# Kernel tuning notes

Hardware: AMD Instinct MI355X
Metric: run time of the kernel (lower is better)

Reference implementation:

```python
import jax, jax.numpy as jnp
import numpy as np

B, N, BS, H, DH, L, FF, V, R = 1, 4096, 64, 12, 64, 4, 3072, 30522, 3
D = H * DH
M = N // BS
NEG = -10000.0


def layernorm(x, g, b, eps=1e-5):
    mu = x.mean(-1, keepdims=True)
    var = ((x - mu) ** 2).mean(-1, keepdims=True)
    return (x - mu) * jax.lax.rsqrt(var + eps) * g + b


def bigbird_attention(q, k, v, band_mask, from_mask, to_mask, blocked_mask, rand_attn):
    # q,k,v: [b,h,n,d]; band_mask [b,1,m-4,BS,3BS]; to_mask [b,1,1,n]; from_mask [b,1,n,1]
    b, h, n, d = q.shape
    m = n // BS
    r = rand_attn.shape[-1]
    sc = 1.0 / jnp.sqrt(jnp.float32(d))
    qb = q.reshape(b, h, m, BS, d)
    kb = k.reshape(b, h, m, BS, d)
    vb = v.reshape(b, h, m, BS, d)
    hid = jnp.arange(h)[:, None, None]
    gk = kb[:, hid, rand_attn].reshape(b, h, m - 2, r * BS, d)  # gathered random keys
    gv = vb[:, hid, rand_attn].reshape(b, h, m - 2, r * BS, d)
    rand_to = blocked_mask[:, rand_attn].reshape(b, h, m - 2, r * BS)
    rand_mask = jnp.einsum('blq,bhlk->bhlqk', blocked_mask[:, 1:-1], rand_to)  # [b,h,m-2,BS,rBS]

    # first block: dense over all keys (global)
    s = jnp.einsum('bhqd,bhkd->bhqk', qb[:, :, 0], k) * sc + (1.0 - to_mask) * NEG
    c_first = jnp.einsum('bhqk,bhkd->bhqd', jax.nn.softmax(s, axis=-1), v)

    # second block: blocks 0,1,2, last, + random row 0
    k2 = jnp.concatenate([kb[:, :, 0], kb[:, :, 1], kb[:, :, 2], kb[:, :, -1], gk[:, :, 0]], axis=2)
    v2 = jnp.concatenate([vb[:, :, 0], vb[:, :, 1], vb[:, :, 2], vb[:, :, -1], gv[:, :, 0]], axis=2)
    s = jnp.einsum('bhqd,bhkd->bhqk', qb[:, :, 1], k2) * sc
    seq_pad = jnp.concatenate([to_mask[..., :3 * BS], to_mask[..., -BS:],
                               jnp.ones((b, 1, 1, r * BS), s.dtype)], axis=3)
    rnd_pad = jnp.concatenate([jnp.ones((b, h, BS, 4 * BS), s.dtype), rand_mask[:, :, 0]], axis=3)
    s = s + (1.0 - jnp.minimum(seq_pad, rnd_pad)) * NEG
    c_second = jnp.einsum('bhqk,bhkd->bhqd', jax.nn.softmax(s, axis=-1), v2)

    # middle blocks: first-global + 3-block band + random + last-global
    mq = qb[:, :, 2:-2]  # [b,h,m-4,BS,d]
    exp_k = jnp.concatenate([kb[:, :, 1:-3], kb[:, :, 2:-2], kb[:, :, 3:-1]], axis=3)
    exp_v = jnp.concatenate([vb[:, :, 1:-3], vb[:, :, 2:-2], vb[:, :, 3:-1]], axis=3)
    inner = jnp.einsum('bhlqd,bhlkd->bhlqk', mq, exp_k) * sc + (1.0 - band_mask) * NEG
    randp = jnp.einsum('bhlqd,bhlkd->bhlqk', mq, gk[:, :, 1:-1]) * sc + (1.0 - rand_mask[:, :, 1:-1]) * NEG
    firstp = jnp.einsum('bhlqd,bhkd->bhlqk', mq, kb[:, :, 0]) * sc + (1.0 - to_mask[:, :, None, :, :BS]) * NEG
    lastp = jnp.einsum('bhlqd,bhkd->bhlqk', mq, kb[:, :, -1]) * sc + (1.0 - to_mask[:, :, None, :, -BS:]) * NEG
    w = jax.nn.softmax(jnp.concatenate([firstp, inner, randp, lastp], axis=-1), axis=-1)
    c_mid = jnp.einsum('bhlqk,bhlkd->bhlqd', w[..., BS:4 * BS], exp_v)
    c_mid = c_mid + jnp.einsum('bhlqk,bhlkd->bhlqd', w[..., 4 * BS:4 * BS + r * BS], gv[:, :, 1:-1])
    c_mid = c_mid + jnp.einsum('bhlqk,bhkd->bhlqd', w[..., :BS], vb[:, :, 0])
    c_mid = c_mid + jnp.einsum('bhlqk,bhkd->bhlqd', w[..., -BS:], vb[:, :, -1])

    # second-to-last block: block 0, last 3 blocks, + random row -1
    k3 = jnp.concatenate([kb[:, :, 0], kb[:, :, -3], kb[:, :, -2], kb[:, :, -1], gk[:, :, -1]], axis=2)
    v3 = jnp.concatenate([vb[:, :, 0], vb[:, :, -3], vb[:, :, -2], vb[:, :, -1], gv[:, :, -1]], axis=2)
    s = jnp.einsum('bhqd,bhkd->bhqk', qb[:, :, -2], k3) * sc
    seq_pad = jnp.concatenate([to_mask[..., :BS], to_mask[..., -3 * BS:],
                               jnp.ones((b, 1, 1, r * BS), s.dtype)], axis=3)
    rnd_pad = jnp.concatenate([jnp.ones((b, h, BS, 4 * BS), s.dtype), rand_mask[:, :, -1]], axis=3)
    s = s + (1.0 - jnp.minimum(seq_pad, rnd_pad)) * NEG
    c_sl = jnp.einsum('bhqk,bhkd->bhqd', jax.nn.softmax(s, axis=-1), v3)

    # last block: dense over all keys (global)
    s = jnp.einsum('bhqd,bhkd->bhqk', qb[:, :, -1], k) * sc + (1.0 - to_mask) * NEG
    c_last = jnp.einsum('bhqk,bhkd->bhqd', jax.nn.softmax(s, axis=-1), v)

    ctx = jnp.concatenate([c_first[:, :, None], c_second[:, :, None], c_mid,
                           c_sl[:, :, None], c_last[:, :, None]], axis=2)
    ctx = ctx.reshape(b, h, n, d) * from_mask
    return ctx.transpose(0, 2, 1, 3).reshape(b, n, h * d)


def forward(input_ids, mask, rand_attn, emb_word, emb_pos, emb_ln_g, emb_ln_b,
            Wq, bq, Wk, bk, Wv, bv, Wo, bo, ln1_g, ln1_b, W1, b1, W2, b2, ln2_g, ln2_b):
    b, n = input_ids.shape
    m = n // BS
    x = emb_word[input_ids] + emb_pos[None, :n]
    x = layernorm(x, emb_ln_g, emb_ln_b)
    blocked_mask = mask.reshape(b, m, BS)
    exp_to = jnp.concatenate([blocked_mask[:, 1:-3], blocked_mask[:, 2:-2], blocked_mask[:, 3:-1]], axis=2)
    band_mask = jnp.einsum('blq,blk->blqk', blocked_mask[:, 2:-2], exp_to)[:, None]
    from_mask = mask.reshape(b, 1, n, 1)
    to_mask = mask.reshape(b, 1, 1, n)
    for i in range(L):
        q = (x @ Wq[i] + bq[i]).reshape(b, n, H, DH).transpose(0, 2, 1, 3)
        k = (x @ Wk[i] + bk[i]).reshape(b, n, H, DH).transpose(0, 2, 1, 3)
        v = (x @ Wv[i] + bv[i]).reshape(b, n, H, DH).transpose(0, 2, 1, 3)
        a = bigbird_attention(q, k, v, band_mask, from_mask, to_mask, blocked_mask, rand_attn)
        a = a @ Wo[i] + bo[i]
        x = layernorm(x + a, ln1_g[i], ln1_b[i])  # dropout is identity in eval
        f = jax.nn.gelu(x @ W1[i] + b1[i], approximate=False) @ W2[i] + b2[i]
        x = layernorm(x + f, ln2_g[i], ln2_b[i])
    return x


def setup_inputs() -> dict:
    key = jax.random.key(0)
    ks = jax.random.split(key, 12)
    s = 0.02
    nrm = lambda k, shape: jax.random.normal(k, shape, jnp.float32) * s
    rng = np.random.default_rng(0)
    rand_attn = jnp.asarray(rng.integers(1, M - 1, size=(H, M - 2, R)), jnp.int32)
    return {
        'input_ids': jax.random.randint(ks[0], (B, N), 0, V),
        'mask': jnp.ones((B, N), jnp.float32),
        'rand_attn': rand_attn,
        'emb_word': nrm(ks[1], (V, D)),
        'emb_pos': nrm(ks[2], (N, D)),
        'emb_ln_g': jnp.ones((D,), jnp.float32), 'emb_ln_b': jnp.zeros((D,), jnp.float32),
        'Wq': nrm(ks[3], (L, D, D)), 'bq': jnp.zeros((L, D), jnp.float32),
        'Wk': nrm(ks[4], (L, D, D)), 'bk': jnp.zeros((L, D), jnp.float32),
        'Wv': nrm(ks[5], (L, D, D)), 'bv': jnp.zeros((L, D), jnp.float32),
        'Wo': nrm(ks[6], (L, D, D)), 'bo': jnp.zeros((L, D), jnp.float32),
        'ln1_g': jnp.ones((L, D), jnp.float32), 'ln1_b': jnp.zeros((L, D), jnp.float32),
        'W1': nrm(ks[7], (L, D, FF)), 'b1': jnp.zeros((L, FF), jnp.float32),
        'W2': nrm(ks[8], (L, FF, D)), 'b2': jnp.zeros((L, D), jnp.float32),
        'ln2_g': jnp.ones((L, D), jnp.float32), 'ln2_b': jnp.zeros((L, D), jnp.float32),
    }


def reference(input_ids, mask, rand_attn, emb_word, emb_pos, emb_ln_g, emb_ln_b,
              Wq, bq, Wk, bk, Wv, bv, Wo, bo, ln1_g, ln1_b, W1, b1, W2, b2, ln2_g, ln2_b):
    return forward(input_ids, mask, rand_attn, emb_word, emb_pos, emb_ln_g, emb_ln_b,
                   Wq, bq, Wk, bk, Wv, bv, Wo, bo, ln1_g, ln1_b, W1, b1, W2, b2, ln2_g, ln2_b)
```

## Files before the change

### kernel.cpp

```cpp
#include <hip/hip_runtime.h>
#include <hip/hip_bf16.h>
#include <math.h>

#define NTOK   4096
#define DMODEL 768
#define NHEAD  12
#define DHEAD  64
#define NLAYER 4
#define DFF    3072
#define NBLK   64
#define NEGC   -10000.0f

using frag8 = __attribute__((ext_vector_type(8))) short;
using f32x4 = __attribute__((ext_vector_type(4))) float;

typedef __attribute__((address_space(3))) void       lds_void;
typedef const __attribute__((address_space(1))) void gbl_void;

__device__ __forceinline__ void gload_lds16(const void* g, void* l) {
  __builtin_amdgcn_global_load_lds((gbl_void*)g, (lds_void*)l, 16, 0, 0);
}

__device__ __forceinline__ float block_sum256(float v) {
  __shared__ float tmp[4];
  #pragma unroll
  for (int o = 32; o > 0; o >>= 1) v += __shfl_down(v, o, 64);
  __syncthreads();
  if ((threadIdx.x & 63) == 0) tmp[threadIdx.x >> 6] = v;
  __syncthreads();
  return tmp[0] + tmp[1] + tmp[2] + tmp[3];
}

__global__ __launch_bounds__(256) void embed_ln_kernel(
    const int* __restrict__ ids, const float* __restrict__ emb_word,
    const float* __restrict__ emb_pos, const float* __restrict__ g,
    const float* __restrict__ b, float* __restrict__ x,
    __hip_bfloat16* __restrict__ xb)
{
  const int n = blockIdx.x;
  const int tid = threadIdx.x;
  const int id = ids[n];
  float v[3];
  #pragma unroll
  for (int j = 0; j < 3; ++j) {
    int d = tid + j * 256;
    v[j] = emb_word[(size_t)id * DMODEL + d] + emb_pos[(size_t)n * DMODEL + d];
  }
  float mu = block_sum256(v[0] + v[1] + v[2]) * (1.0f / DMODEL);
  float var = 0.f;
  #pragma unroll
  for (int j = 0; j < 3; ++j) { float t = v[j] - mu; var += t * t; }
  var = block_sum256(var) * (1.0f / DMODEL);
  float rs = rsqrtf(var + 1e-5f);
  #pragma unroll
  for (int j = 0; j < 3; ++j) {
    int d = tid + j * 256;
    float o = (v[j] - mu) * rs * g[d] + b[d];
    x[(size_t)n * DMODEL + d] = o;
    xb[(size_t)n * DMODEL + d] = (__hip_bfloat16)o;
  }
}

__global__ __launch_bounds__(256) void add_ln_red_kernel(
    const float* __restrict__ xin, const float* __restrict__ P, size_t ps,
    int nparts, const float* __restrict__ bias2,
    const float* __restrict__ g, const float* __restrict__ b,
    float* __restrict__ dst, __hip_bfloat16* __restrict__ dstb)
{
  const int n = blockIdx.x;
  const int tid = threadIdx.x;
  float v[3];
  #pragma unroll
  for (int j = 0; j < 3; ++j) {
    int d = tid + j * 256;
    float s = xin[(size_t)n * DMODEL + d] + bias2[d];
    for (int z = 0; z < nparts; ++z)
      s += P[(size_t)z * ps + (size_t)n * DMODEL + d];
    v[j] = s;
  }
  float mu = block_sum256(v[0] + v[1] + v[2]) * (1.0f / DMODEL);
  float var = 0.f;
  #pragma unroll
  for (int j = 0; j < 3; ++j) { float t = v[j] - mu; var += t * t; }
  var = block_sum256(var) * (1.0f / DMODEL);
  float rs = rsqrtf(var + 1e-5f);
  #pragma unroll
  for (int j = 0; j < 3; ++j) {
    int d = tid + j * 256;
    float ov = (v[j] - mu) * rs * g[d] + b[d];
    dst[(size_t)n * DMODEL + d] = ov;
    dstb[(size_t)n * DMODEL + d] = (__hip_bfloat16)ov;
  }
}

__global__ __launch_bounds__(256) void prep_weights_kernel(
    const float* __restrict__ Wq, const float* __restrict__ Wk,
    const float* __restrict__ Wv, const float* __restrict__ Wo,
    const float* __restrict__ W1, const float* __restrict__ W2,
    const float* __restrict__ bq, const float* __restrict__ bk,
    const float* __restrict__ bv,
    __hip_bfloat16* __restrict__ wqkvT, __hip_bfloat16* __restrict__ woT,
    __hip_bfloat16* __restrict__ w1T, __hip_bfloat16* __restrict__ w2T,
    float* __restrict__ biasf)
{
  const int id = blockIdx.x;
  if (id >= 6912) {
    int t = (id - 6912) * 256 + threadIdx.x;
    if (t < 3 * DMODEL)
      biasf[t] = (t < DMODEL) ? bq[t] : (t < 2 * DMODEL ? bk[t - DMODEL] : bv[t - 2 * DMODEL]);
    return;
  }
  const float* src;
  __hip_bfloat16* dst;
  int K, N, local;
  if (id < 2304) {
    int m = id / 576; local = id % 576;
    src = (m == 0) ? Wq : (m == 1) ? Wk : (m == 2) ? Wv : Wo;
    dst = (m < 3) ? wqkvT + (size_t)m * DMODEL * DMODEL : woT;
    K = DMODEL; N = DMODEL;
  } else if (id < 4608) {
    local = id - 2304; src = W1; dst = w1T; K = DMODEL; N = DFF;
  } else {
    local = id - 4608; src = W2; dst = w2T; K = DFF; N = DMODEL;
  }
  const int ntiles = N / 32;
  const int n0 = (local % ntiles) * 32;
  const int k0 = (local / ntiles) * 32;

  __shared__ float tile[32][33];
  const int c = threadIdx.x & 31;
  const int r0 = threadIdx.x >> 5;
  #pragma unroll
  for (int i = 0; i < 4; ++i) {
    int r = r0 + i * 8;
    tile[r][c] = src[(size_t)(k0 + r) * N + n0 + c];
  }
  __syncthreads();
  #pragma unroll
  for (int i = 0; i < 4; ++i) {
    int r = r0 + i * 8;
    dst[(size_t)(n0 + r) * K + k0 + c] = (__hip_bfloat16)tile[c][r];
  }
}

__global__ __launch_bounds__(256) void gemm_bf16_kernel(
    const __hip_bfloat16* __restrict__ A, int lda,
    const __hip_bfloat16* __restrict__ BT, int ldb,
    const float* __restrict__ bias,
    float* __restrict__ Cf, size_t cfStride,
    __hip_bfloat16* __restrict__ Cb,
    int Kpart, int ldC, int do_gelu)
{
  __shared__ __hip_bfloat16 Als[2][64 * 32];
  __shared__ __hip_bfloat16 Bls[2][128 * 32];
  const int tid = threadIdx.x;

  const int gx = gridDim.x;
  const int nwg = gx * gridDim.y;
  const int orig = blockIdx.y * gx + blockIdx.x;
  const int q = nwg >> 3, r = nwg & 7;
  const int xcd = orig & 7, loc = orig >> 3;
  const int wg = (xcd < r ? xcd * (q + 1) : r * (q + 1) + (xcd - r) * q) + loc;
  const int bm = (wg % gx) * 64;
  const int bn = (wg / gx) * 128;
  const int z  = blockIdx.z;
  const int koff = z * Kpart;

  const int wave = tid >> 6, lane = tid & 63;
  const int wm = (wave >> 1) * 32, wn = (wave & 1) * 64;
  const int lm = lane & 15, quad = lane >> 4;

  const int rA = wave * 16 + (lane >> 2);
  const int kc = (lane & 3) * 8;

  const __hip_bfloat16* Ar  = A  + (size_t)(bm + rA) * lda + koff + kc;
  const __hip_bfloat16* Br0 = BT + (size_t)(bn + rA) * ldb + koff + kc;
  const __hip_bfloat16* Br1 = BT + (size_t)(bn + 64 + rA) * ldb + koff + kc;

  f32x4 acc[2][4];
  #pragma unroll
  for (int i = 0; i < 2; ++i)
    #pragma unroll
    for (int j = 0; j < 4; ++j)
      acc[i][j] = (f32x4){0.f, 0.f, 0.f, 0.f};

  gload_lds16(Ar,  &Als[0][rA * 32 + kc]);
  gload_lds16(Br0, &Bls[0][rA * 32 + kc]);
  gload_lds16(Br1, &Bls[0][(64 + rA) * 32 + kc]);

  int p = 0;
  for (int k0 = 0; k0 < Kpart; k0 += 32, p ^= 1) {
    __syncthreads();
    const int kn = k0 + 32;
    if (kn < Kpart) {
      gload_lds16(Ar + kn,  &Als[p ^ 1][rA * 32 + kc]);
      gload_lds16(Br0 + kn, &Bls[p ^ 1][rA * 32 + kc]);
      gload_lds16(Br1 + kn, &Bls[p ^ 1][(64 + rA) * 32 + kc]);
    }
    frag8 afr[2], bfr[4];
    #pragma unroll
    for (int t = 0; t < 2; ++t)
      afr[t] = *(const frag8*)(&Als[p][(wm + t * 16 + lm) * 32 + quad * 8]);
    #pragma unroll
    for (int nt = 0; nt < 4; ++nt)
      bfr[nt] = *(const frag8*)(&Bls[p][(wn + nt * 16 + lm) * 32 + quad * 8]);
    #pragma unroll
    for (int mt = 0; mt < 2; ++mt)
      #pragma unroll
      for (int nt = 0; nt < 4; ++nt)
        acc[mt][nt] = __builtin_amdgcn_mfma_f32_16x16x32_bf16(
            afr[mt], bfr[nt], acc[mt][nt], 0, 0, 0);
  }

  float* Cfz = Cf ? Cf + (size_t)z * cfStride : nullptr;
  #pragma unroll
  for (int mt = 0; mt < 2; ++mt)
    #pragma unroll
    for (int nt = 0; nt < 4; ++nt)
      #pragma unroll
      for (int rr = 0; rr < 4; ++rr) {
        int row = bm + wm + mt * 16 + quad * 4 + rr;
        int col = bn + wn + nt * 16 + lm;
        float v = acc[mt][nt][rr];
        if (bias) v += bias[col];
        if (do_gelu) v = 0.5f * v * (1.f + erff(v * 0.70710678118654752f));
        if (Cfz) Cfz[(size_t)row * ldC + col] = v;
        if (Cb) Cb[(size_t)row * ldC + col] = (__hip_bfloat16)v;
      }
}

__global__ __launch_bounds__(512, 2) void gemm256_kernel(
    const __hip_bfloat16* __restrict__ A, int lda,
    const __hip_bfloat16* __restrict__ BT,
    const float* __restrict__ bias,
    __hip_bfloat16* __restrict__ Cb, int ldC,
    int K, int do_gelu)
{
  __shared__ uint4 smem4[131072 / 16];
  char* lds = (char*)smem4;
  const int tid = threadIdx.x;
  const int bm = blockIdx.x * 256;
  const int bn = blockIdx.y * 256;
  const int wave = tid >> 6, lane = tid & 63;
  const int wm = wave >> 2;
  const int wn = wave & 3;
  const int lm = lane & 15, quad = lane >> 4;

  const int srow = tid >> 3;
  const int schx = ((tid & 7) ^ (srow & 7)) * 16;
  const int ldst0 = tid * 16;
  const int ldst1 = 8192 + tid * 16;
  const char* Abytes = (const char*)A;
  const char* Bbytes = (const char*)BT;
  const size_t ldab = (size_t)lda * 2;

  const int co0 = ((0 + quad) ^ (lm & 7)) * 16;
  const int co1 = ((4 + quad) ^ (lm & 7)) * 16;

  f32x4 acc[8][4];
  #pragma unroll
  for (int i = 0; i < 8; ++i)
    #pragma unroll
    for (int j = 0; j < 4; ++j)
      acc[i][j] = (f32x4){0.f, 0.f, 0.f, 0.f};

#define STAGE(BASE, ROW0, LOFF, KB) do {                                      \
    const char* _s = (BASE) + (size_t)((ROW0) + srow) * ldab + (KB) + schx;   \
    gload_lds16(_s, lds + (LOFF) + ldst0);                                    \
    gload_lds16(_s + 64 * ldab, lds + (LOFF) + ldst1);                        \
  } while (0)

  STAGE(Abytes, bm,        0,             (size_t)0);
  STAGE(Abytes, bm + 128,  16384,         (size_t)0);
  STAGE(Bbytes, bn,        65536,         (size_t)0);
  STAGE(Bbytes, bn + 128,  65536 + 16384, (size_t)0);

  frag8 a[4][2], b[2][2];

#define RD_A(MTB) do {                                                        \
    _Pragma("unroll")                                                         \
    for (int mt = 0; mt < 4; ++mt) {                                          \
      const char* ap = Ab + (size_t)((wm * 128 + ((MTB) + mt) * 16 + lm) * 128); \
      a[mt][0] = *(const frag8*)(ap + co0);                                   \
      a[mt][1] = *(const frag8*)(ap + co1);                                   \
    } } while (0)
#define RD_B(NTB) do {                                                        \
    _Pragma("unroll")                                                         \
    for (int nt = 0; nt < 2; ++nt) {                                          \
      const char* bp = Bb + (size_t)((wn * 64 + ((NTB) + nt) * 16 + lm) * 128); \
      b[nt][0] = *(const frag8*)(bp + co0);                                   \
      b[nt][1] = *(const frag8*)(bp + co1);                                   \
    } } while (0)
#define MMQ(MTB, NTB) do {                                                    \
    _Pragma("unroll")                                                         \
    for (int mt = 0; mt < 4; ++mt)                                            \
      _Pragma("unroll")                                                       \
      for (int nt = 0; nt < 2; ++nt) {                                        \
        acc[(MTB) + mt][(NTB) + nt] = __builtin_amdgcn_mfma_f32_16x16x32_bf16( \
            a[mt][0], b[nt][0], acc[(MTB) + mt][(NTB) + nt], 0, 0, 0);        \
        acc[(MTB) + mt][(NTB) + nt] = __builtin_amdgcn_mfma_f32_16x16x32_bf16( \
            a[mt][1], b[nt][1], acc[(MTB) + mt][(NTB) + nt], 0, 0, 0);        \
      } } while (0)

  const int NT = K >> 6;
  for (int t = 0; t < NT; ++t) {
    const int p = t & 1;
    const char* Ab = lds + p * 32768;
    const char* Bb = lds + 65536 + p * 32768;
    const int qb_ = (p ^ 1) * 32768;
    const size_t kb = (size_t)(t + 1) * 128;
    const bool more = (t + 1 < NT);

    if (more) {
      STAGE(Abytes, bm, qb_, kb);
      asm volatile("s_waitcnt vmcnt(2)" ::: "memory");
    } else {
      asm volatile("s_waitcnt vmcnt(0)" ::: "memory");
    }
    __builtin_amdgcn_sched_barrier(0);
    __builtin_amdgcn_s_barrier();
    __builtin_amdgcn_sched_barrier(0);
    RD_A(0); RD_B(0);
    __builtin_amdgcn_s_setprio(1);
    MMQ(0, 0);
    __builtin_amdgcn_s_setprio(0);
    __builtin_amdgcn_s_barrier();

    RD_B(2);
    if (more) STAGE(Abytes, bm + 128, qb_ + 16384, kb);
    __builtin_amdgcn_s_barrier();
    __builtin_amdgcn_s_setprio(1);
    MMQ(0, 2);
    __builtin_amdgcn_s_setprio(0);
    __builtin_amdgcn_s_barrier();

    RD_A(4);
    if (more) STAGE(Bbytes, bn, 65536 + qb_, kb);
    __builtin_amdgcn_s_barrier();
    __builtin_amdgcn_s_setprio(1);
    MMQ(4, 2);
    __builtin_amdgcn_s_setprio(0);
    __builtin_amdgcn_s_barrier();

    RD_B(0);
    if (more) STAGE(Bbytes, bn + 128, 65536 + qb_ + 16384, kb);
    __builtin_amdgcn_s_barrier();
    __builtin_amdgcn_s_setprio(1);
    MMQ(4, 0);
    __builtin_amdgcn_s_setprio(0);
    __builtin_amdgcn_s_barrier();
  }

#undef STAGE
#undef RD_A
#undef RD_B
#undef MMQ

  #pragma unroll
  for (int mt = 0; mt < 8; ++mt)
    #pragma unroll
    for (int nt = 0; nt < 4; ++nt)
      #pragma unroll
      for (int rr = 0; rr < 4; ++rr) {
        int row = bm + wm * 128 + mt * 16 + quad * 4 + rr;
        int col = bn + wn * 64 + nt * 16 + lm;
        float v = acc[mt][nt][rr] + bias[col];
        if (do_gelu) v = 0.5f * v * (1.f + erff(v * 0.70710678118654752f));
        Cb[(size_t)row * ldC + col] = (__hip_bfloat16)v;
      }
}

__global__ __launch_bounds__(256) void attn_kernel(
    const __hip_bfloat16* __restrict__ qkvb, const float* __restrict__ mask,
    const int* __restrict__ rand_attn, __hip_bfloat16* __restrict__ outp,
    float* __restrict__ Mpart, float* __restrict__ Lpart, float* __restrict__ Opart)
{
  const int h = blockIdx.x;
  const int item = blockIdx.y;
  const int tid = threadIdx.x;

  int qi, chunk;
  if (item < 8)       { qi = 0;        chunk = item; }
  else if (item < 70) { qi = item - 7; chunk = -1; }
  else                { qi = 63;       chunk = item - 70; }

  __shared__ __hip_bfloat16 Qs[64 * 72];
  __shared__ __hip_bfloat16 Ks[64 * 72];
  __shared__ __hip_bfloat16 VTs[64 * 72];
  __shared__ __hip_bfloat16 Ps[64 * 72];
  __shared__ int slist[8];
  __shared__ int snb;

  const __hip_bfloat16* qg = qkvb;
  const __hip_bfloat16* kg = qkvb + DMODEL;
  const __hip_bfloat16* vg = qkvb + 2 * DMODEL;
  const int ldq = 3 * DMODEL;

  const int wave = tid >> 6, lane = tid & 63;
  const int wm = wave * 16;
  const int lm = lane & 15, quad = lane >> 4;

  {
    int r = tid >> 2, c0 = (tid & 3) * 16;
    const __hip_bfloat16* qp = qg + (size_t)(qi * 64 + r) * ldq + h * 64 + c0;
    uint4 a = *(const uint4*)qp;
    uint4 b = *(const uint4*)(qp + 8);
    *(uint4*)(Qs + r * 72 + c0) = a;
    *(uint4*)(Qs + r * 72 + c0 + 8) = b;
  }
  if (tid == 0) {
    if (chunk >= 0) {
      for (int j = 0; j < 8; ++j) slist[j] = chunk * 8 + j;
      snb = 8;
    } else {
      const int* ra = rand_attn + ((size_t)h * 62 + (qi - 1)) * 3;
      if (qi == 1)       { slist[0] = 0; slist[1] = 1;  slist[2] = 2;  slist[3] = 63; }
      else if (qi == 62) { slist[0] = 0; slist[1] = 61; slist[2] = 62; slist[3] = 63; }
      else               { slist[0] = 0; slist[1] = qi - 1; slist[2] = qi; slist[3] = qi + 1; }
      slist[4] = ra[0]; slist[5] = ra[1]; slist[6] = ra[2];
      int nb = 7;
      if (qi >= 2 && qi <= 61) { slist[7] = 63; nb = 8; }
      snb = nb;
    }
  }
  __syncthreads();
  const int nb = snb;

  frag8 aq0 = *(const frag8*)(Qs + (wm + lm) * 72 + quad * 8);
  frag8 aq1 = *(const frag8*)(Qs + (wm + lm) * 72 + 32 + quad * 8);

  float mold[4], lsum[4];
  #pragma unroll
  for (int r = 0; r < 4; ++r) { mold[r] = -1e30f; lsum[r] = 0.f; }
  f32x4 oacc[4];
  #pragma unroll
  for (int t = 0; t < 4; ++t) oacc[t] = (f32x4){0.f, 0.f, 0.f, 0.f};

  const int sr = tid >> 2, sc0 = (tid & 3) * 16;

  for (int bi = 0; bi < nb; ++bi) {
    const int kb = slist[bi];
    const __hip_bfloat16* kp = kg + (size_t)(kb * 64 + sr) * ldq + h * 64 + sc0;
    const __hip_bfloat16* vp = vg + (size_t)(kb * 64 + sr) * ldq + h * 64 + sc0;
    uint4 kv0 = *(const uint4*)kp;
    uint4 kv1 = *(const uint4*)(kp + 8);
    uint4 vv0 = *(const uint4*)vp;
    uint4 vv1 = *(const uint4*)(vp + 8);
    float msk[4];
    #pragma unroll
    for (int t = 0; t < 4; ++t) msk[t] = mask[kb * 64 + t * 16 + lm];

    __syncthreads();
    *(uint4*)(Ks + sr * 72 + sc0) = kv0;
    *(uint4*)(Ks + sr * 72 + sc0 + 8) = kv1;
    {
      union { uint4 u[2]; __hip_bfloat16 h16[16]; } vu;
      vu.u[0] = vv0; vu.u[1] = vv1;
      #pragma unroll
      for (int j = 0; j < 16; ++j)
        VTs[(sc0 + j) * 72 + sr] = vu.h16[j];
    }
    __syncthreads();

    f32x4 sacc[4];
    #pragma unroll
    for (int t = 0; t < 4; ++t) sacc[t] = (f32x4){0.f, 0.f, 0.f, 0.f};
    #pragma unroll
    for (int t = 0; t < 4; ++t) {
      frag8 bk0 = *(const frag8*)(Ks + (t * 16 + lm) * 72 + quad * 8);
      frag8 bk1 = *(const frag8*)(Ks + (t * 16 + lm) * 72 + 32 + quad * 8);
      sacc[t] = __builtin_amdgcn_mfma_f32_16x16x32_bf16(aq0, bk0, sacc[t], 0, 0, 0);
      sacc[t] = __builtin_amdgcn_mfma_f32_16x16x32_bf16(aq1, bk1, sacc[t], 0, 0, 0);
    }

    float xs[4][4];
    #pragma unroll
    for (int t = 0; t < 4; ++t)
      #pragma unroll
      for (int r = 0; r < 4; ++r)
        xs[t][r] = sacc[t][r] * 0.125f + (1.f - msk[t]) * NEGC;

    float al[4], psum[4];
    #pragma unroll
    for (int r = 0; r < 4; ++r) {
      float rm = fmaxf(fmaxf(xs[0][r], xs[1][r]), fmaxf(xs[2][r], xs[3][r]));
      rm = fmaxf(rm, __shfl_xor(rm, 1, 64));
      rm = fmaxf(rm, __shfl_xor(rm, 2, 64));
      rm = fmaxf(rm, __shfl_xor(rm, 4, 64));
      rm = fmaxf(rm, __shfl_xor(rm, 8, 64));
      float mnew = fmaxf(mold[r], rm);
      al[r] = __expf(mold[r] - mnew);
      float s = 0.f;
      #pragma unroll
      for (int t = 0; t < 4; ++t) {
        float p = __expf(xs[t][r] - mnew);
        xs[t][r] = p;
        s += p;
      }
      s += __shfl_xor(s, 1, 64);
      s += __shfl_xor(s, 2, 64);
      s += __shfl_xor(s, 4, 64);
      s += __shfl_xor(s, 8, 64);
      psum[r] = s;
      mold[r] = mnew;
    }
    #pragma unroll
    for (int r = 0; r < 4; ++r) lsum[r] = lsum[r] * al[r] + psum[r];
    #pragma unroll
    for (int t = 0; t < 4; ++t)
      #pragma unroll
      for (int r = 0; r < 4; ++r)
        oacc[t][r] *= al[r];

    #pragma unroll
    for (int t = 0; t < 4; ++t)
      #pragma unroll
      for (int r = 0; r < 4; ++r)
        Ps[(wm + quad * 4 + r) * 72 + t * 16 + lm] = (__hip_bfloat16)xs[t][r];

    frag8 ap0 = *(const frag8*)(Ps + (wm + lm) * 72 + quad * 8);
    frag8 ap1 = *(const frag8*)(Ps + (wm + lm) * 72 + 32 + quad * 8);
    #pragma unroll
    for (int t = 0; t < 4; ++t) {
      frag8 bv0 = *(const frag8*)(VTs + (t * 16 + lm) * 72 + quad * 8);
      frag8 bv1 = *(const frag8*)(VTs + (t * 16 + lm) * 72 + 32 + quad * 8);
      oacc[t] = __builtin_amdgcn_mfma_f32_16x16x32_bf16(ap0, bv0, oacc[t], 0, 0, 0);
      oacc[t] = __builtin_amdgcn_mfma_f32_16x16x32_bf16(ap1, bv1, oacc[t], 0, 0, 0);
    }
  }

  if (chunk < 0) {
    #pragma unroll
    for (int r = 0; r < 4; ++r) {
      int row = qi * 64 + wm + quad * 4 + r;
      float sc2 = mask[row] / lsum[r];
      #pragma unroll
      for (int t = 0; t < 4; ++t)
        outp[(size_t)row * DMODEL + h * 64 + t * 16 + lm] =
            (__hip_bfloat16)(oacc[t][r] * sc2);
    }
  } else {
    const int idx = (h * 2 + (qi == 63 ? 1 : 0)) * 8 + chunk;
    #pragma unroll
    for (int r = 0; r < 4; ++r) {
      int row = wm + quad * 4 + r;
      #pragma unroll
      for (int t = 0; t < 4; ++t)
        Opart[(size_t)idx * 4096 + row * 64 + t * 16 + lm] = oacc[t][r];
      if (lm == 0) {
        Mpart[idx * 64 + row] = mold[r];
        Lpart[idx * 64 + row] = lsum[r];
      }
    }
  }
}

__global__ __launch_bounds__(256) void attn_merge_kernel(
    const float* __restrict__ Mpart, const float* __restrict__ Lpart,
    const float* __restrict__ Opart, const float* __restrict__ mask,
    __hip_bfloat16* __restrict__ outp)
{
  const int h = blockIdx.x, side = blockIdx.y;
  const int qi = side ? 63 : 0;
  const int tid = threadIdx.x;
  const int r = tid >> 2;
  const int d0 = (tid & 3) * 16;
  const int base = (h * 2 + side) * 8;

  float mv[8], m = -1e30f;
  #pragma unroll
  for (int c = 0; c < 8; ++c) { mv[c] = Mpart[(base + c) * 64 + r]; m = fmaxf(m, mv[c]); }
  float sc[8], l = 0.f;
  #pragma unroll
  for (int c = 0; c < 8; ++c) {
    sc[c] = __expf(mv[c] - m);
    l += Lpart[(base + c) * 64 + r] * sc[c];
  }
  float o[16];
  #pragma unroll
  for (int d = 0; d < 16; ++d) o[d] = 0.f;
  #pragma unroll
  for (int c = 0; c < 8; ++c) {
    const float* Op = Opart + (size_t)(base + c) * 4096 + r * 64 + d0;
    #pragma unroll
    for (int d4 = 0; d4 < 4; ++d4) {
      float4 v4 = *(const float4*)(Op + d4 * 4);
      o[d4 * 4 + 0] += v4.x * sc[c];
      o[d4 * 4 + 1] += v4.y * sc[c];
      o[d4 * 4 + 2] += v4.z * sc[c];
      o[d4 * 4 + 3] += v4.w * sc[c];
    }
  }
  const int row = qi * 64 + r;
  float inv = mask[row] / l;
  #pragma unroll
  for (int d = 0; d < 16; ++d)
    outp[(size_t)row * DMODEL + h * 64 + d0 + d] = (__hip_bfloat16)(o[d] * inv);
}

extern "C" void kernel_launch(void* const* d_in, const int* in_sizes, int n_in,
                              void* d_out, int out_size, void* d_ws, size_t ws_size,
                              hipStream_t stream)
{
  const int*   ids      = (const int*)  d_in[0];
  const float* mask     = (const float*)d_in[1];
  const int*   rand_att = (const int*)  d_in[2];
  const float* emb_word = (const float*)d_in[3];
  const float* emb_pos  = (const float*)d_in[4];
  const float* eg       = (const float*)d_in[5];
  const float* eb       = (const float*)d_in[6];
  const float* Wq = (const float*)d_in[7];
  const float* bq = (const float*)d_in[8];
  const float* Wk = (const float*)d_in[9];
  const float* bk = (const float*)d_in[10];
  const float* Wv = (const float*)d_in[11];
  const float* bv = (const float*)d_in[12];
  const float* Wo = (const float*)d_in[13];
  const float* bo = (const float*)d_in[14];
  const float* ln1g = (const float*)d_in[15];
  const float* ln1b = (const float*)d_in[16];
  const float* W1 = (const float*)d_in[17];
  const float* bf1 = (const float*)d_in[18];
  const float* W2 = (const float*)d_in[19];
  const float* bf2 = (const float*)d_in[20];
  const float* ln2g = (const float*)d_in[21];
  const float* ln2b = (const float*)d_in[22];

  const size_t ND = (size_t)NTOK * DMODEL;
  float* x   = (float*)d_ws;
  __hip_bfloat16* xb = (__hip_bfloat16*)(x + ND);
  float* P   = (float*)(xb + ND);
  __hip_bfloat16* qkvb = (__hip_bfloat16*)(P + 3 * ND);
  __hip_bfloat16* fb_b = qkvb + 3 * ND;
  __hip_bfloat16* ab_b = fb_b + (size_t)NTOK * DFF;
  __hip_bfloat16* wqkvT = ab_b + ND;
  __hip_bfloat16* woT  = wqkvT + (size_t)3 * DMODEL * DMODEL;
  __hip_bfloat16* w1T  = woT  + (size_t)DMODEL * DMODEL;
  __hip_bfloat16* w2T  = w1T  + (size_t)DFF * DMODEL;
  float* biasf = (float*)(w2T + (size_t)DMODEL * DFF);
  float* Mpart = biasf + 3 * DMODEL;
  float* Lpart = Mpart + NHEAD * 2 * 8 * 64;
  float* Opart = Lpart + NHEAD * 2 * 8 * 64;

  embed_ln_kernel<<<NTOK, 256, 0, stream>>>(ids, emb_word, emb_pos, eg, eb, x, xb);

  for (int l = 0; l < NLAYER; ++l) {
    const float* Wq_l = Wq + (size_t)l * DMODEL * DMODEL;
    const float* Wk_l = Wk + (size_t)l * DMODEL * DMODEL;
    const float* Wv_l = Wv + (size_t)l * DMODEL * DMODEL;
    const float* Wo_l = Wo + (size_t)l * DMODEL * DMODEL;
    const float* W1_l = W1 + (size_t)l * DMODEL * DFF;
    const float* W2_l = W2 + (size_t)l * DFF * DMODEL;

    prep_weights_kernel<<<6921, 256, 0, stream>>>(
        Wq_l, Wk_l, Wv_l, Wo_l, W1_l, W2_l,
        bq + (size_t)l * DMODEL, bk + (size_t)l * DMODEL, bv + (size_t)l * DMODEL,
        wqkvT, woT, w1T, w2T, biasf);

    gemm256_kernel<<<dim3(NTOK / 256, 3 * DMODEL / 256), 512, 0, stream>>>(
        xb, DMODEL, wqkvT, biasf, qkvb, 3 * DMODEL, DMODEL, 0);

    attn_kernel<<<dim3(NHEAD, 78), 256, 0, stream>>>(qkvb, mask, rand_att, ab_b,
                                                     Mpart, Lpart, Opart);
    attn_merge_kernel<<<dim3(NHEAD, 2), 256, 0, stream>>>(Mpart, Lpart, Opart, mask, ab_b);

    gemm_bf16_kernel<<<dim3(NTOK / 64, DMODEL / 128, 2), 256, 0, stream>>>(
        ab_b, DMODEL, woT, DMODEL, nullptr, P, ND, nullptr, DMODEL / 2, DMODEL, 0);
    add_ln_red_kernel<<<NTOK, 256, 0, stream>>>(x, P, ND, 2, bo + (size_t)l * DMODEL,
                                                ln1g + (size_t)l * DMODEL,
                                                ln1b + (size_t)l * DMODEL, x, xb);

    gemm256_kernel<<<dim3(NTOK / 256, DFF / 256), 512, 0, stream>>>(
        xb, DMODEL, w1T, bf1 + (size_t)l * DFF, fb_b, DFF, DMODEL, 1);

    gemm_bf16_kernel<<<dim3(NTOK / 64, DMODEL / 128, 3), 256, 0, stream>>>(
        fb_b, DFF, w2T, DFF, nullptr, P, ND, nullptr, DFF / 3, DMODEL, 0);
    add_ln_red_kernel<<<NTOK, 256, 0, stream>>>(x, P, ND, 3, bf2 + (size_t)l * DMODEL,
                                                ln2g + (size_t)l * DMODEL,
                                                ln2b + (size_t)l * DMODEL,
                                                (l == NLAYER - 1) ? (float*)d_out : x, xb);
  }
}
```

Baseline: 1.084 ms.

## Route Wo and W2 projections through 256x256 GEMM with split-K over four slices

Removes the 64x128-tile GEMM kernel and generalises the 256x256 swizzled GEMM to support split-K, optional bias and fp32 partial outputs. The attention output projection and the second FFN projection now use the large-tile kernel with four K partitions, and the residual/LayerNorm kernel reduces four partials. The aim is more data reuse per workgroup and higher MFMA efficiency than the small-tile path. In exchange, each of these GEMMs launches only 192 workgroups, which may leave CUs idle, and it writes and reads an extra fp32 partial buffer. The attention projection also gets a very short K loop per slice.

```diff
diff --git a/kernel.cpp b/kernel.cpp
--- a/kernel.cpp
+++ b/kernel.cpp
@@ -143,104 +143,20 @@
   }
 }
 
-__global__ __launch_bounds__(256) void gemm_bf16_kernel(
-    const __hip_bfloat16* __restrict__ A, int lda,
-    const __hip_bfloat16* __restrict__ BT, int ldb,
+__global__ __launch_bounds__(512, 2) void gemm256_kernel(
+    const __hip_bfloat16* __restrict__ A, int ld,
+    const __hip_bfloat16* __restrict__ BT,
     const float* __restrict__ bias,
     float* __restrict__ Cf, size_t cfStride,
-    __hip_bfloat16* __restrict__ Cb,
-    int Kpart, int ldC, int do_gelu)
-{
-  __shared__ __hip_bfloat16 Als[2][64 * 32];
-  __shared__ __hip_bfloat16 Bls[2][128 * 32];
-  const int tid = threadIdx.x;
-
-  const int gx = gridDim.x;
-  const int nwg = gx * gridDim.y;
-  const int orig = blockIdx.y * gx + blockIdx.x;
-  const int q = nwg >> 3, r = nwg & 7;
-  const int xcd = orig & 7, loc = orig >> 3;
-  const int wg = (xcd < r ? xcd * (q + 1) : r * (q + 1) + (xcd - r) * q) + loc;
-  const int bm = (wg % gx) * 64;
-  const int bn = (wg / gx) * 128;
-  const int z  = blockIdx.z;
-  const int koff = z * Kpart;
-
-  const int wave = tid >> 6, lane = tid & 63;
-  const int wm = (wave >> 1) * 32, wn = (wave & 1) * 64;
-  const int lm = lane & 15, quad = lane >> 4;
-
-  const int rA = wave * 16 + (lane >> 2);
-  const int kc = (lane & 3) * 8;
-
-  const __hip_bfloat16* Ar  = A  + (size_t)(bm + rA) * lda + koff + kc;
-  const __hip_bfloat16* Br0 = BT + (size_t)(bn + rA) * ldb + koff + kc;
-  const __hip_bfloat16* Br1 = BT + (size_t)(bn + 64 + rA) * ldb + koff + kc;
-
-  f32x4 acc[2][4];
-  #pragma unroll
-  for (int i = 0; i < 2; ++i)
-    #pragma unroll
-    for (int j = 0; j < 4; ++j)
-      acc[i][j] = (f32x4){0.f, 0.f, 0.f, 0.f};
-
-  gload_lds16(Ar,  &Als[0][rA * 32 + kc]);
-  gload_lds16(Br0, &Bls[0][rA * 32 + kc]);
-  gload_lds16(Br1, &Bls[0][(64 + rA) * 32 + kc]);
-
-  int p = 0;
-  for (int k0 = 0; k0 < Kpart; k0 += 32, p ^= 1) {
-    __syncthreads();
-    const int kn = k0 + 32;
-    if (kn < Kpart) {
-      gload_lds16(Ar + kn,  &Als[p ^ 1][rA * 32 + kc]);
-      gload_lds16(Br0 + kn, &Bls[p ^ 1][rA * 32 + kc]);
-      gload_lds16(Br1 + kn, &Bls[p ^ 1][(64 + rA) * 32 + kc]);
-    }
-    frag8 afr[2], bfr[4];
-    #pragma unroll
-    for (int t = 0; t < 2; ++t)
-      afr[t] = *(const frag8*)(&Als[p][(wm + t * 16 + lm) * 32 + quad * 8]);
-    #pragma unroll
-    for (int nt = 0; nt < 4; ++nt)
-      bfr[nt] = *(const frag8*)(&Bls[p][(wn + nt * 16 + lm) * 32 + quad * 8]);
-    #pragma unroll
-    for (int mt = 0; mt < 2; ++mt)
-      #pragma unroll
-      for (int nt = 0; nt < 4; ++nt)
-        acc[mt][nt] = __builtin_amdgcn_mfma_f32_16x16x32_bf16(
-            afr[mt], bfr[nt], acc[mt][nt], 0, 0, 0);
-  }
-
-  float* Cfz = Cf ? Cf + (size_t)z * cfStride : nullptr;
-  #pragma unroll
-  for (int mt = 0; mt < 2; ++mt)
-    #pragma unroll
-    for (int nt = 0; nt < 4; ++nt)
-      #pragma unroll
-      for (int rr = 0; rr < 4; ++rr) {
-        int row = bm + wm + mt * 16 + quad * 4 + rr;
-        int col = bn + wn + nt * 16 + lm;
-        float v = acc[mt][nt][rr];
-        if (bias) v += bias[col];
-        if (do_gelu) v = 0.5f * v * (1.f + erff(v * 0.70710678118654752f));
-        if (Cfz) Cfz[(size_t)row * ldC + col] = v;
-        if (Cb) Cb[(size_t)row * ldC + col] = (__hip_bfloat16)v;
-      }
-}
-
-__global__ __launch_bounds__(512, 2) void gemm256_kernel(
-    const __hip_bfloat16* __restrict__ A, int lda,
-    const __hip_bfloat16* __restrict__ BT,
-    const float* __restrict__ bias,
     __hip_bfloat16* __restrict__ Cb, int ldC,
-    int K, int do_gelu)
+    int Kpart, int do_gelu)
 {
   __shared__ uint4 smem4[131072 / 16];
   char* lds = (char*)smem4;
   const int tid = threadIdx.x;
   const int bm = blockIdx.x * 256;
   const int bn = blockIdx.y * 256;
+  const int z  = blockIdx.z;
   const int wave = tid >> 6, lane = tid & 63;
   const int wm = wave >> 2;
   const int wn = wave & 3;
@@ -250,9 +166,10 @@
   const int schx = ((tid & 7) ^ (srow & 7)) * 16;
   const int ldst0 = tid * 16;
   const int ldst1 = 8192 + tid * 16;
-  const char* Abytes = (const char*)A;
-  const char* Bbytes = (const char*)BT;
-  const size_t ldab = (size_t)lda * 2;
+  const size_t koffb = (size_t)z * Kpart * 2;
+  const char* Abytes = (const char*)A + koffb;
+  const char* Bbytes = (const char*)BT + koffb;
+  const size_t ldab = (size_t)ld * 2;
 
   const int co0 = ((0 + quad) ^ (lm & 7)) * 16;
   const int co1 = ((4 + quad) ^ (lm & 7)) * 16;
@@ -302,7 +219,7 @@
             a[mt][1], b[nt][1], acc[(MTB) + mt][(NTB) + nt], 0, 0, 0);        \
       } } while (0)
 
-  const int NT = K >> 6;
+  const int NT = Kpart >> 6;
   for (int t = 0; t < NT; ++t) {
     const int p = t & 1;
     const char* Ab = lds + p * 32768;
@@ -356,6 +273,7 @@
 #undef RD_B
 #undef MMQ
 
+  float* Cfz = Cf ? Cf + (size_t)z * cfStride : nullptr;
   #pragma unroll
   for (int mt = 0; mt < 8; ++mt)
     #pragma unroll
@@ -364,9 +282,11 @@
       for (int rr = 0; rr < 4; ++rr) {
         int row = bm + wm * 128 + mt * 16 + quad * 4 + rr;
         int col = bn + wn * 64 + nt * 16 + lm;
-        float v = acc[mt][nt][rr] + bias[col];
+        float v = acc[mt][nt][rr];
+        if (bias) v += bias[col];
         if (do_gelu) v = 0.5f * v * (1.f + erff(v * 0.70710678118654752f));
-        Cb[(size_t)row * ldC + col] = (__hip_bfloat16)v;
+        if (Cfz) Cfz[(size_t)row * ldC + col] = v;
+        if (Cb) Cb[(size_t)row * ldC + col] = (__hip_bfloat16)v;
       }
 }
 
@@ -630,7 +550,7 @@
   float* x   = (float*)d_ws;
   __hip_bfloat16* xb = (__hip_bfloat16*)(x + ND);
   float* P   = (float*)(xb + ND);
-  __hip_bfloat16* qkvb = (__hip_bfloat16*)(P + 3 * ND);
+  __hip_bfloat16* qkvb = (__hip_bfloat16*)(P + 4 * ND);
   __hip_bfloat16* fb_b = qkvb + 3 * ND;
   __hip_bfloat16* ab_b = fb_b + (size_t)NTOK * DFF;
   __hip_bfloat16* wqkvT = ab_b + ND;
@@ -658,24 +578,24 @@
         wqkvT, woT, w1T, w2T, biasf);
 
     gemm256_kernel<<<dim3(NTOK / 256, 3 * DMODEL / 256), 512, 0, stream>>>(
-        xb, DMODEL, wqkvT, biasf, qkvb, 3 * DMODEL, DMODEL, 0);
+        xb, DMODEL, wqkvT, biasf, nullptr, 0, qkvb, 3 * DMODEL, DMODEL, 0);
 
     attn_kernel<<<dim3(NHEAD, 78), 256, 0, stream>>>(qkvb, mask, rand_att, ab_b,
                                                      Mpart, Lpart, Opart);
     attn_merge_kernel<<<dim3(NHEAD, 2), 256, 0, stream>>>(Mpart, Lpart, Opart, mask, ab_b);
 
-    gemm_bf16_kernel<<<dim3(NTOK / 64, DMODEL / 128, 2), 256, 0, stream>>>(
-        ab_b, DMODEL, woT, DMODEL, nullptr, P, ND, nullptr, DMODEL / 2, DMODEL, 0);
-    add_ln_red_kernel<<<NTOK, 256, 0, stream>>>(x, P, ND, 2, bo + (size_t)l * DMODEL,
+    gemm256_kernel<<<dim3(NTOK / 256, DMODEL / 256, 4), 512, 0, stream>>>(
+        ab_b, DMODEL, woT, nullptr, P, ND, nullptr, DMODEL, DMODEL / 4, 0);
+    add_ln_red_kernel<<<NTOK, 256, 0, stream>>>(x, P, ND, 4, bo + (size_t)l * DMODEL,
                                                 ln1g + (size_t)l * DMODEL,
                                                 ln1b + (size_t)l * DMODEL, x, xb);
 
     gemm256_kernel<<<dim3(NTOK / 256, DFF / 256), 512, 0, stream>>>(
-        xb, DMODEL, w1T, bf1 + (size_t)l * DFF, fb_b, DFF, DMODEL, 1);
-
-    gemm_bf16_kernel<<<dim3(NTOK / 64, DMODEL / 128, 3), 256, 0, stream>>>(
-        fb_b, DFF, w2T, DFF, nullptr, P, ND, nullptr, DFF / 3, DMODEL, 0);
-    add_ln_red_kernel<<<NTOK, 256, 0, stream>>>(x, P, ND, 3, bf2 + (size_t)l * DMODEL,
+        xb, DMODEL, w1T, bf1 + (size_t)l * DFF, nullptr, 0, fb_b, DFF, DMODEL, 1);
+
+    gemm256_kernel<<<dim3(NTOK / 256, DMODEL / 256, 4), 512, 0, stream>>>(
+        fb_b, DFF, w2T, nullptr, P, ND, nullptr, DMODEL, DFF / 4, 0);
+    add_ln_red_kernel<<<NTOK, 256, 0, stream>>>(x, P, ND, 4, bf2 + (size_t)l * DMODEL,
                                                 ln2g + (size_t)l * DMODEL,
                                                 ln2b + (size_t)l * DMODEL,
                                                 (l == NLAYER - 1) ? (float*)d_out : x, xb);
```

New measurement: 1.190 ms. 9.8% more time.
